# Kernel optimization log

Measured on AMD Instinct MI355X. Metric: run time of the kernel, lower is better.

Reference implementation:

```python
import jax, jax.numpy as jnp
import numpy as np

N_NODES = 50000
N_EDGES = 800000
HIDDEN = 128
EDGE_DIM = 16
N_HEADS = 8
HEAD_DIM = HIDDEN // N_HEADS
SCALE = 1.0 / np.sqrt(HEAD_DIM).astype(np.float32)
LN_EPS = 1e-5


def setup_inputs() -> dict:
    key = jax.random.key(0)
    ks = jax.random.split(key, 24)
    s = 0.02

    def w(k, shape):
        return jax.random.normal(k, shape, dtype=jnp.float32) * s

    inp = {
        "node_features": jax.random.normal(ks[0], (N_NODES, HIDDEN), dtype=jnp.float32),
        "edge_index": jax.random.randint(ks[1], (2, N_EDGES), 0, N_NODES, dtype=jnp.int32),
        "edge_features": jax.random.normal(ks[2], (N_EDGES, EDGE_DIM), dtype=jnp.float32),
        # projections stored as [in, out] (y = x @ W + b)
        "Wq": w(ks[3], (HIDDEN, HIDDEN)), "bq": jnp.zeros((HIDDEN,), jnp.float32),
        "Wk": w(ks[4], (HIDDEN, HIDDEN)), "bk": jnp.zeros((HIDDEN,), jnp.float32),
        "Wv": w(ks[5], (HIDDEN, HIDDEN)), "bv": jnp.zeros((HIDDEN,), jnp.float32),
        "Wb1": w(ks[6], (EDGE_DIM, N_HEADS)), "bb1": jnp.zeros((N_HEADS,), jnp.float32),
        "Wb2": w(ks[7], (N_HEADS, N_HEADS)), "bb2": jnp.zeros((N_HEADS,), jnp.float32),
        "Wo": w(ks[8], (HIDDEN, HIDDEN)), "bo": jnp.zeros((HIDDEN,), jnp.float32),
        "Wf1": w(ks[9], (HIDDEN, 2 * HIDDEN)), "bf1": jnp.zeros((2 * HIDDEN,), jnp.float32),
        "Wf2": w(ks[10], (2 * HIDDEN, HIDDEN)), "bf2": jnp.zeros((HIDDEN,), jnp.float32),
        "g1": jnp.ones((HIDDEN,), jnp.float32), "be1": jnp.zeros((HIDDEN,), jnp.float32),
        "g2": jnp.ones((HIDDEN,), jnp.float32), "be2": jnp.zeros((HIDDEN,), jnp.float32),
    }
    return inp


def _layer_norm(x, gamma, beta):
    mu = jnp.mean(x, axis=-1, keepdims=True)
    var = jnp.mean(jnp.square(x - mu), axis=-1, keepdims=True)
    return (x - mu) * jax.lax.rsqrt(var + LN_EPS) * gamma + beta


def reference(node_features, edge_index, edge_features,
              Wq, bq, Wk, bk, Wv, bv, Wb1, bb1, Wb2, bb2,
              Wo, bo, Wf1, bf1, Wf2, bf2, g1, be1, g2, be2):
    n_nodes = node_features.shape[0]
    src, dst = edge_index[0], edge_index[1]

    q = (node_features @ Wq + bq).reshape(n_nodes, N_HEADS, HEAD_DIM)
    k = (node_features @ Wk + bk).reshape(n_nodes, N_HEADS, HEAD_DIM)
    v = (node_features @ Wv + bv).reshape(n_nodes, N_HEADS, HEAD_DIM)

    # per-edge attention logits [E, H]
    edge_bias = jax.nn.silu(edge_features @ Wb1 + bb1) @ Wb2 + bb2
    logits = jnp.sum(q[dst] * k[src], axis=-1) * SCALE + edge_bias

    # segment softmax over edges sharing the same dst node
    max_s = jax.ops.segment_max(logits, dst, num_segments=n_nodes)
    exp_s = jnp.exp(logits - max_s[dst])
    norm = jax.ops.segment_sum(exp_s, dst, num_segments=n_nodes)
    attn = exp_s / jnp.clip(norm[dst], 1e-12)

    # weighted aggregation [N, H, D] -> [N, hidden]
    weighted = attn[:, :, None] * v[src]
    aggregated = jax.ops.segment_sum(weighted, dst, num_segments=n_nodes)
    aggregated = aggregated.reshape(n_nodes, HIDDEN)

    x = _layer_norm(node_features + (aggregated @ Wo + bo), g1, be1)
    ffn = jax.nn.silu(x @ Wf1 + bf1) @ Wf2 + bf2
    return _layer_norm(x + ffn, g2, be2)
```

## Files before the change

### kernel.cpp

```cpp
#include <hip/hip_runtime.h>
#include <hip/hip_bf16.h>
#include <math.h>

#define HIDDEN 128
#define EDGE_DIM 16
#define N_HEADS 8
#define QK_SCALE 0.25f
#define LN_EPS 1e-5f

using bf16x8 = __attribute__((ext_vector_type(8))) short;
using f32x4 = __attribute__((ext_vector_type(4))) float;
typedef __hip_bfloat16 bf16;

__device__ __forceinline__ float b2f(short u) {
  union { unsigned int i; float f; } c;
  c.i = ((unsigned int)(unsigned short)u) << 16;
  return c.f;
}
__device__ __forceinline__ short f2b(float f) {
  bf16 h = __float2bfloat16(f);
  union { bf16 b; short s; } c;
  c.b = h;
  return c.s;
}

__global__ __launch_bounds__(256) void conv_weights_kernel(
    const float* __restrict__ Wq, const float* __restrict__ Wk, const float* __restrict__ Wv,
    const float* __restrict__ bq, const float* __restrict__ bk, const float* __restrict__ bv,
    const float* __restrict__ Wo, const float* __restrict__ Wf1, const float* __restrict__ Wf2,
    bf16* __restrict__ Wqkv_t, bf16* __restrict__ Wo_t, bf16* __restrict__ Wf1_t,
    bf16* __restrict__ Wf2_t, float* __restrict__ bqkv) {
  int i = blockIdx.x * 256 + threadIdx.x;
  if (i < 49152) {
    int n = i >> 7, k = i & 127;
    const float* W = (n < 128) ? Wq : ((n < 256) ? Wk : Wv);
    int nn = n & 127;
    Wqkv_t[i] = __float2bfloat16(W[k * 128 + nn]);
  } else if (i < 65536) {
    int j = i - 49152;
    int n = j >> 7, k = j & 127;
    Wo_t[j] = __float2bfloat16(Wo[k * 128 + n]);
  } else if (i < 98304) {
    int j = i - 65536;
    int n = j >> 7, k = j & 127;
    Wf1_t[j] = __float2bfloat16(Wf1[k * 256 + n]);
  } else if (i < 131072) {
    int j = i - 98304;
    int n = j >> 8, k = j & 255;
    Wf2_t[j] = __float2bfloat16(Wf2[k * 128 + n]);
  }
  if (i < 384) bqkv[i] = (i < 128) ? bq[i] : ((i < 256) ? bk[i - 128] : bv[i - 256]);
}

template <int K, int EPI, int OUTBF, int AF32>
__global__ __launch_bounds__(256) void mfma_gemm_kernel(
    const void* __restrict__ Ap, const bf16* __restrict__ Wt,
    const float* __restrict__ bias, void* __restrict__ Cout, int M, int Nc) {
  const int tid = threadIdx.x;
  const int w = tid >> 6, l = tid & 63;
  const int wr = w >> 1, wc = w & 1;
  const int lr = l & 15, lk = l >> 4;
  const int bm = blockIdx.x * 64;
  const int bn = blockIdx.y * 128 + wc * 64;

  f32x4 acc[2][4] = {};
  const int arow0 = bm + wr * 32 + lr;

  for (int k0 = 0; k0 < K; k0 += 128) {
    bf16x8 bfr[4][4];
#pragma unroll
    for (int fn = 0; fn < 4; ++fn) {
      const bf16* wp = Wt + (size_t)(bn + fn * 16 + lr) * K + k0 + lk * 8;
#pragma unroll
      for (int ks = 0; ks < 4; ++ks) bfr[fn][ks] = *(const bf16x8*)(wp + ks * 32);
    }
    bf16x8 afr[2][4];
#pragma unroll
    for (int fr = 0; fr < 2; ++fr) {
      int row = arow0 + fr * 16;
      if (row >= M) row = M - 1;
      if (AF32) {
        const float* ap = (const float*)Ap + (size_t)row * K + k0 + lk * 8;
#pragma unroll
        for (int ks = 0; ks < 4; ++ks) {
          float4 x = *(const float4*)(ap + ks * 32);
          float4 y = *(const float4*)(ap + ks * 32 + 4);
          bf16x8 t;
          t[0] = f2b(x.x); t[1] = f2b(x.y); t[2] = f2b(x.z); t[3] = f2b(x.w);
          t[4] = f2b(y.x); t[5] = f2b(y.y); t[6] = f2b(y.z); t[7] = f2b(y.w);
          afr[fr][ks] = t;
        }
      } else {
        const bf16* ap = (const bf16*)Ap + (size_t)row * K + k0 + lk * 8;
#pragma unroll
        for (int ks = 0; ks < 4; ++ks) afr[fr][ks] = *(const bf16x8*)(ap + ks * 32);
      }
    }
#pragma unroll
    for (int ks = 0; ks < 4; ++ks)
#pragma unroll
      for (int fr = 0; fr < 2; ++fr)
#pragma unroll
        for (int fn = 0; fn < 4; ++fn)
          acc[fr][fn] = __builtin_amdgcn_mfma_f32_16x16x32_bf16(afr[fr][ks], bfr[fn][ks],
                                                                acc[fr][fn], 0, 0, 0);
  }

#pragma unroll
  for (int fn = 0; fn < 4; ++fn) {
    const int col = bn + fn * 16 + lr;
    const float bv = bias[col];
#pragma unroll
    for (int fr = 0; fr < 2; ++fr) {
      const int rbase = bm + wr * 32 + fr * 16 + lk * 4;
#pragma unroll
      for (int r = 0; r < 4; ++r) {
        int row = rbase + r;
        if (row < M) {
          float o = acc[fr][fn][r] + bv;
          if (EPI == 1) o = o / (1.f + __expf(-o));
          if (OUTBF)
            ((bf16*)Cout)[(size_t)row * Nc + col] = __float2bfloat16(o);
          else
            ((float*)Cout)[(size_t)row * Nc + col] = o;
        }
      }
    }
  }
}

template <int K>
__global__ __launch_bounds__(256) void mfma_gemm_ln_kernel(
    const bf16* __restrict__ A, const bf16* __restrict__ Wt,
    const float* __restrict__ bias, const float* __restrict__ R,
    const float* __restrict__ gam, const float* __restrict__ bet,
    float* __restrict__ y, bf16* __restrict__ yb, int M) {
  const int tid = threadIdx.x;
  const int w = tid >> 6, l = tid & 63;
  const int wr = w >> 1, wc = w & 1;
  const int lr = l & 15, lk = l >> 4;
  const int bm = blockIdx.x * 64;
  const int bn = wc * 64;

  f32x4 acc[2][4] = {};
  const int arow0 = bm + wr * 32 + lr;

  for (int k0 = 0; k0 < K; k0 += 128) {
    bf16x8 bfr[4][4];
#pragma unroll
    for (int fn = 0; fn < 4; ++fn) {
      const bf16* wp = Wt + (size_t)(bn + fn * 16 + lr) * K + k0 + lk * 8;
#pragma unroll
      for (int ks = 0; ks < 4; ++ks) bfr[fn][ks] = *(const bf16x8*)(wp + ks * 32);
    }
    bf16x8 afr[2][4];
#pragma unroll
    for (int fr = 0; fr < 2; ++fr) {
      int row = arow0 + fr * 16;
      if (row >= M) row = M - 1;
      const bf16* ap = A + (size_t)row * K + k0 + lk * 8;
#pragma unroll
      for (int ks = 0; ks < 4; ++ks) afr[fr][ks] = *(const bf16x8*)(ap + ks * 32);
    }
#pragma unroll
    for (int ks = 0; ks < 4; ++ks)
#pragma unroll
      for (int fr = 0; fr < 2; ++fr)
#pragma unroll
        for (int fn = 0; fn < 4; ++fn)
          acc[fr][fn] = __builtin_amdgcn_mfma_f32_16x16x32_bf16(afr[fr][ks], bfr[fn][ks],
                                                                acc[fr][fn], 0, 0, 0);
  }

  float bv[4], gv[4], ev[4];
#pragma unroll
  for (int fn = 0; fn < 4; ++fn) {
    int col = bn + fn * 16 + lr;
    bv[fn] = bias[col];
    gv[fn] = gam[col];
    ev[fn] = bet[col];
  }
  float ps[2][4], psq[2][4];
#pragma unroll
  for (int fr = 0; fr < 2; ++fr) {
#pragma unroll
    for (int r = 0; r < 4; ++r) {
      int row = bm + wr * 32 + fr * 16 + lk * 4 + r;
      int rrow = (row < M) ? row : (M - 1);
      float s = 0.f, sq = 0.f;
#pragma unroll
      for (int fn = 0; fn < 4; ++fn) {
        int col = bn + fn * 16 + lr;
        float o = acc[fr][fn][r] + bv[fn] + R[(size_t)rrow * HIDDEN + col];
        acc[fr][fn][r] = o;
        s += o;
        sq += o * o;
      }
      ps[fr][r] = s;
      psq[fr][r] = sq;
    }
  }
#pragma unroll
  for (int off = 1; off < 16; off <<= 1) {
#pragma unroll
    for (int fr = 0; fr < 2; ++fr)
#pragma unroll
      for (int r = 0; r < 4; ++r) {
        ps[fr][r] += __shfl_xor(ps[fr][r], off, 64);
        psq[fr][r] += __shfl_xor(psq[fr][r], off, 64);
      }
  }
  __shared__ float s_sum[2][64], s_sq[2][64];
  if (lr == 0) {
#pragma unroll
    for (int fr = 0; fr < 2; ++fr)
#pragma unroll
      for (int r = 0; r < 4; ++r) {
        int rl = wr * 32 + fr * 16 + lk * 4 + r;
        s_sum[wc][rl] = ps[fr][r];
        s_sq[wc][rl] = psq[fr][r];
      }
  }
  __syncthreads();
#pragma unroll
  for (int fr = 0; fr < 2; ++fr) {
#pragma unroll
    for (int r = 0; r < 4; ++r) {
      int rl = wr * 32 + fr * 16 + lk * 4 + r;
      int row = bm + rl;
      float tot = s_sum[0][rl] + s_sum[1][rl];
      float tsq = s_sq[0][rl] + s_sq[1][rl];
      float mean = tot * (1.f / 128.f);
      float var = tsq * (1.f / 128.f) - mean * mean;
      float rstd = rsqrtf(var + LN_EPS);
      if (row < M) {
#pragma unroll
        for (int fn = 0; fn < 4; ++fn) {
          int col = bn + fn * 16 + lr;
          float val = (acc[fr][fn][r] - mean) * rstd * gv[fn] + ev[fn];
          if (y) y[(size_t)row * HIDDEN + col] = val;
          if (yb) yb[(size_t)row * HIDDEN + col] = __float2bfloat16(val);
        }
      }
    }
  }
}

__global__ void hist_kernel(const int* __restrict__ dst, int* __restrict__ counts, int E) {
  int e = blockIdx.x * blockDim.x + threadIdx.x;
  if (e < E) atomicAdd(&counts[dst[e]], 1);
}

__device__ __forceinline__ int wave_incl_scan(int x, int lane) {
  int incl = x;
#pragma unroll
  for (int off = 1; off < 64; off <<= 1) {
    int y = __shfl_up(incl, off, 64);
    if (lane >= off) incl += y;
  }
  return incl;
}

__global__ __launch_bounds__(256) void scan_block_kernel(const int* __restrict__ counts,
                                                         int* __restrict__ offs,
                                                         int* __restrict__ btot, int N) {
  __shared__ int s4[4];
  int tid = threadIdx.x;
  int i = blockIdx.x * 256 + tid;
  int lane = tid & 63, wv = tid >> 6;
  int x = (i < N) ? counts[i] : 0;
  int incl = wave_incl_scan(x, lane);
  if (lane == 63) s4[wv] = incl;
  __syncthreads();
  if (tid == 0) {
    int s = 0;
#pragma unroll
    for (int j = 0; j < 4; ++j) { int t = s4[j]; s4[j] = s; s += t; }
    btot[blockIdx.x] = s;
  }
  __syncthreads();
  if (i < N) offs[i] = s4[wv] + incl - x;
}

__global__ __launch_bounds__(256) void scan_tot_kernel(int* __restrict__ btot, int nb) {
  __shared__ int s4[4];
  __shared__ int carry;
  int tid = threadIdx.x;
  int lane = tid & 63, wv = tid >> 6;
  if (tid == 0) carry = 0;
  __syncthreads();
  for (int c0 = 0; c0 < nb; c0 += 256) {
    int i = c0 + tid;
    int x = (i < nb) ? btot[i] : 0;
    int incl = wave_incl_scan(x, lane);
    if (lane == 63) s4[wv] = incl;
    __syncthreads();
    if (tid == 0) {
      int s = 0;
#pragma unroll
      for (int j = 0; j < 4; ++j) { int t = s4[j]; s4[j] = s; s += t; }
    }
    __syncthreads();
    int base = carry + s4[wv];
    if (i < nb) btot[i] = base + incl - x;
    __syncthreads();
    if (tid == 255) carry = base + incl;
    __syncthreads();
  }
}

__global__ __launch_bounds__(256) void scan_add_kernel(int* __restrict__ offs,
                                                       const int* __restrict__ btot,
                                                       int N, int E) {
  int i = blockIdx.x * 256 + threadIdx.x;
  if (i < N) offs[i] += btot[blockIdx.x];
  if (i == 0) offs[N] = E;
}

__global__ __launch_bounds__(256) void scatter_mlp_kernel(
    const int* __restrict__ dst, const int* __restrict__ src,
    const float* __restrict__ ef, const float* __restrict__ Wb1,
    const float* __restrict__ bb1, const float* __restrict__ Wb2,
    const float* __restrict__ bb2, const int* __restrict__ offs,
    int* __restrict__ cursor, int* __restrict__ src_csr,
    bf16* __restrict__ ebw, int E) {
  __shared__ float w1[128], w2[64], b1[8], b2[8];
  int tid = threadIdx.x;
  if (tid < 128) w1[tid] = Wb1[tid];
  else if (tid < 192) w2[tid - 128] = Wb2[tid - 128];
  else if (tid < 200) b1[tid - 192] = bb1[tid - 192];
  else if (tid < 208) b2[tid - 200] = bb2[tid - 200];
  __syncthreads();

  int e = blockIdx.x * 256 + tid;
  if (e >= E) return;

  const float4* p4 = (const float4*)(ef + (size_t)e * 16);
  float4 f0 = p4[0], f1 = p4[1], f2 = p4[2], f3 = p4[3];
  float x[16] = {f0.x, f0.y, f0.z, f0.w, f1.x, f1.y, f1.z, f1.w,
                 f2.x, f2.y, f2.z, f2.w, f3.x, f3.y, f3.z, f3.w};

  float h[8];
#pragma unroll
  for (int j = 0; j < 8; ++j) h[j] = b1[j];
#pragma unroll
  for (int i = 0; i < 16; ++i) {
    float xi = x[i];
#pragma unroll
    for (int j = 0; j < 8; ++j) h[j] = fmaf(xi, w1[i * 8 + j], h[j]);
  }
#pragma unroll
  for (int j = 0; j < 8; ++j) h[j] = h[j] / (1.f + __expf(-h[j]));

  float o[8];
#pragma unroll
  for (int j = 0; j < 8; ++j) o[j] = b2[j];
#pragma unroll
  for (int jj = 0; jj < 8; ++jj) {
    float hj = h[jj];
#pragma unroll
    for (int j = 0; j < 8; ++j) o[j] = fmaf(hj, w2[jj * 8 + j], o[j]);
  }
  bf16x8 o8;
#pragma unroll
  for (int j = 0; j < 8; ++j) o8[j] = f2b(o[j]);

  int d = dst[e];
  int p = offs[d] + atomicAdd(&cursor[d], 1);
  src_csr[p] = src[e];
  *(bf16x8*)(ebw + (size_t)p * 8) = o8;
}

__global__ __launch_bounds__(256) void node_attn_kernel(
    const bf16* __restrict__ qkv, const int* __restrict__ src_csr,
    const bf16* __restrict__ ebw, const int* __restrict__ offs,
    bf16* __restrict__ agg, int Nn) {
  int n = blockIdx.x * 4 + (threadIdx.x >> 6);
  if (n >= Nn) return;
  int l = threadIdx.x & 63;
  int g = l >> 4;
  int il = l & 15;
  int head = il >> 1;

  bf16x8 q8 = *(const bf16x8*)(qkv + (size_t)n * 384 + il * 8);
  float qf[8];
#pragma unroll
  for (int j = 0; j < 8; ++j) qf[j] = b2f(q8[j]) * QK_SCALE;

  int s0 = offs[n], s1 = offs[n + 1];
  float lsum = 0.f;
  float acc[8] = {};

  for (int p0 = s0; p0 < s1; p0 += 4) {
    int p = p0 + g;
    bool valid = p < s1;
    int pc = valid ? p : s1 - 1;
    int s = src_csr[pc];
    float ebv = b2f(ebw[(size_t)pc * 8 + head]);
    const bf16* kvrow = qkv + (size_t)s * 384 + 128;
    bf16x8 k8 = *(const bf16x8*)(kvrow + il * 8);
    bf16x8 v8 = *(const bf16x8*)(kvrow + 128 + il * 8);

    float prod = 0.f;
#pragma unroll
    for (int j = 0; j < 8; ++j) prod = fmaf(qf[j], b2f(k8[j]), prod);
    prod += __shfl_xor(prod, 1, 64);

    float pe = valid ? __expf(prod + ebv) : 0.f;
    lsum += pe;
#pragma unroll
    for (int j = 0; j < 8; ++j) acc[j] = fmaf(pe, b2f(v8[j]), acc[j]);
  }

#pragma unroll
  for (int off = 16; off < 64; off <<= 1) {
    lsum += __shfl_xor(lsum, off, 64);
#pragma unroll
    for (int j = 0; j < 8; ++j) acc[j] += __shfl_xor(acc[j], off, 64);
  }

  if (g == 0) {
    float inv = (lsum > 0.f) ? 1.f / lsum : 0.f;
    bf16x8 o8;
#pragma unroll
    for (int j = 0; j < 8; ++j) o8[j] = f2b(acc[j] * inv);
    *(bf16x8*)(agg + (size_t)n * HIDDEN + il * 8) = o8;
  }
}

extern "C" void kernel_launch(void* const* d_in, const int* in_sizes, int n_in,
                              void* d_out, int out_size, void* d_ws, size_t ws_size,
                              hipStream_t stream) {
  const float* nf = (const float*)d_in[0];
  const int* ei = (const int*)d_in[1];
  const float* ef = (const float*)d_in[2];
  const float* Wq = (const float*)d_in[3];
  const float* bq = (const float*)d_in[4];
  const float* Wk = (const float*)d_in[5];
  const float* bk_ = (const float*)d_in[6];
  const float* Wv = (const float*)d_in[7];
  const float* bv = (const float*)d_in[8];
  const float* Wb1 = (const float*)d_in[9];
  const float* bb1 = (const float*)d_in[10];
  const float* Wb2 = (const float*)d_in[11];
  const float* bb2 = (const float*)d_in[12];
  const float* Wo = (const float*)d_in[13];
  const float* bo = (const float*)d_in[14];
  const float* Wf1 = (const float*)d_in[15];
  const float* bf1 = (const float*)d_in[16];
  const float* Wf2 = (const float*)d_in[17];
  const float* bf2 = (const float*)d_in[18];
  const float* g1 = (const float*)d_in[19];
  const float* be1 = (const float*)d_in[20];
  const float* g2 = (const float*)d_in[21];
  const float* be2 = (const float*)d_in[22];

  const int N = in_sizes[0] / HIDDEN;
  const int E = in_sizes[2] / EDGE_DIM;
  const int* srcA = ei;
  const int* dstA = ei + E;

  char* base = (char*)d_ws;
  size_t off = 0;
  auto alloc = [&](size_t bytes) {
    off = (off + 255) & ~(size_t)255;
    char* p = base + off;
    off += bytes;
    return p;
  };

  bf16* qkv = (bf16*)alloc((size_t)N * 384 * 2);
  bf16* hbuf = qkv;
  bf16* agg = (bf16*)alloc((size_t)N * HIDDEN * 2);
  float* x1 = (float*)alloc((size_t)N * HIDDEN * 4);
  bf16* x1b = (bf16*)alloc((size_t)N * HIDDEN * 2);
  int* src_csr = (int*)alloc((size_t)E * 4);
  bf16* ebw = (bf16*)alloc((size_t)E * N_HEADS * 2);
  int* counts = (int*)alloc((size_t)N * 4);
  int* offs = (int*)alloc((size_t)(N + 1) * 4);
  int* cursor = (int*)alloc((size_t)N * 4);
  const int nb = (N + 255) / 256;
  int* btot = (int*)alloc((size_t)nb * 4);
  bf16* Wqkv_t = (bf16*)alloc(384 * 128 * 2);
  bf16* Wo_t = (bf16*)alloc(128 * 128 * 2);
  bf16* Wf1_t = (bf16*)alloc(256 * 128 * 2);
  bf16* Wf2_t = (bf16*)alloc(128 * 256 * 2);
  float* bqkv = (float*)alloc(384 * 4);

  float* outp = (float*)d_out;
  const int mb64 = (N + 63) / 64;
  const int eblocks = (E + 255) / 256;

  conv_weights_kernel<<<512, 256, 0, stream>>>(Wq, Wk, Wv, bq, bk_, bv, Wo, Wf1, Wf2,
                                               Wqkv_t, Wo_t, Wf1_t, Wf2_t, bqkv);

  mfma_gemm_kernel<128, 0, 1, 1><<<dim3(mb64, 3), 256, 0, stream>>>(
      nf, Wqkv_t, bqkv, qkv, N, 384);

  hipMemsetAsync(counts, 0, (size_t)N * 4, stream);
  hipMemsetAsync(cursor, 0, (size_t)N * 4, stream);
  hist_kernel<<<eblocks, 256, 0, stream>>>(dstA, counts, E);
  scan_block_kernel<<<nb, 256, 0, stream>>>(counts, offs, btot, N);
  scan_tot_kernel<<<1, 256, 0, stream>>>(btot, nb);
  scan_add_kernel<<<nb, 256, 0, stream>>>(offs, btot, N, E);
  scatter_mlp_kernel<<<eblocks, 256, 0, stream>>>(dstA, srcA, ef, Wb1, bb1, Wb2, bb2,
                                                  offs, cursor, src_csr, ebw, E);

  node_attn_kernel<<<(N + 3) / 4, 256, 0, stream>>>(qkv, src_csr, ebw, offs, agg, N);

  mfma_gemm_ln_kernel<128><<<mb64, 256, 0, stream>>>(agg, Wo_t, bo, nf, g1, be1, x1, x1b, N);

  mfma_gemm_kernel<128, 1, 1, 0><<<dim3(mb64, 2), 256, 0, stream>>>(
      x1b, Wf1_t, bf1, hbuf, N, 256);

  mfma_gemm_ln_kernel<256><<<mb64, 256, 0, stream>>>(hbuf, Wf2_t, bf2, x1, g2, be2,
                                                     outp, nullptr, N);
}
```

Baseline: 298.4 us.

## Store edge bias in edge order, widen per-lane head work, swap GEMM grid axes

The edge-bias MLP output is now written with coalesced nontemporal stores in original edge order, and the CSR stores (src, edge id) pairs so the attention kernel can gather the bias by edge id. Before, the bias was scattered to random CSR positions. The attention kernel now gives each lane a full head of 16 dims, processing 8 edges per iteration. This drops the intra-head shuffle but adds more shuffle steps for the final reduction and a random gather of the bias. GEMM grids are transposed so consecutive blocks share A rows, and the counts and cursor memsets are merged into one.

```diff
diff --git a/kernel.cpp b/kernel.cpp
--- a/kernel.cpp
+++ b/kernel.cpp
@@ -10,6 +10,7 @@
 
 using bf16x8 = __attribute__((ext_vector_type(8))) short;
 using f32x4 = __attribute__((ext_vector_type(4))) float;
+using f32x4v = __attribute__((ext_vector_type(4))) float;
 typedef __hip_bfloat16 bf16;
 
 __device__ __forceinline__ float b2f(short u) {
@@ -60,8 +61,8 @@
   const int w = tid >> 6, l = tid & 63;
   const int wr = w >> 1, wc = w & 1;
   const int lr = l & 15, lk = l >> 4;
-  const int bm = blockIdx.x * 64;
-  const int bn = blockIdx.y * 128 + wc * 64;
+  const int bm = blockIdx.y * 64;
+  const int bn = blockIdx.x * 128 + wc * 64;
 
   f32x4 acc[2][4] = {};
   const int arow0 = bm + wr * 32 + lr;
@@ -322,8 +323,8 @@
     const float* __restrict__ ef, const float* __restrict__ Wb1,
     const float* __restrict__ bb1, const float* __restrict__ Wb2,
     const float* __restrict__ bb2, const int* __restrict__ offs,
-    int* __restrict__ cursor, int* __restrict__ src_csr,
-    bf16* __restrict__ ebw, int E) {
+    int* __restrict__ cursor, int2* __restrict__ es_csr,
+    bf16* __restrict__ eb, int E) {
   __shared__ float w1[128], w2[64], b1[8], b2[8];
   int tid = threadIdx.x;
   if (tid < 128) w1[tid] = Wb1[tid];
@@ -335,10 +336,13 @@
   int e = blockIdx.x * 256 + tid;
   if (e >= E) return;
 
-  const float4* p4 = (const float4*)(ef + (size_t)e * 16);
-  float4 f0 = p4[0], f1 = p4[1], f2 = p4[2], f3 = p4[3];
-  float x[16] = {f0.x, f0.y, f0.z, f0.w, f1.x, f1.y, f1.z, f1.w,
-                 f2.x, f2.y, f2.z, f2.w, f3.x, f3.y, f3.z, f3.w};
+  const f32x4v* p4 = (const f32x4v*)(ef + (size_t)e * 16);
+  f32x4v f0 = __builtin_nontemporal_load(p4 + 0);
+  f32x4v f1 = __builtin_nontemporal_load(p4 + 1);
+  f32x4v f2 = __builtin_nontemporal_load(p4 + 2);
+  f32x4v f3 = __builtin_nontemporal_load(p4 + 3);
+  float x[16] = {f0[0], f0[1], f0[2], f0[3], f1[0], f1[1], f1[2], f1[3],
+                 f2[0], f2[1], f2[2], f2[3], f3[0], f3[1], f3[2], f3[3]};
 
   float h[8];
 #pragma unroll
@@ -364,67 +368,82 @@
   bf16x8 o8;
 #pragma unroll
   for (int j = 0; j < 8; ++j) o8[j] = f2b(o[j]);
+  __builtin_nontemporal_store(o8, (bf16x8*)(eb + (size_t)e * 8));
 
   int d = dst[e];
   int p = offs[d] + atomicAdd(&cursor[d], 1);
-  src_csr[p] = src[e];
-  *(bf16x8*)(ebw + (size_t)p * 8) = o8;
+  es_csr[p] = make_int2(src[e], e);
 }
 
 __global__ __launch_bounds__(256) void node_attn_kernel(
-    const bf16* __restrict__ qkv, const int* __restrict__ src_csr,
-    const bf16* __restrict__ ebw, const int* __restrict__ offs,
+    const bf16* __restrict__ qkv, const int2* __restrict__ es_csr,
+    const bf16* __restrict__ eb, const int* __restrict__ offs,
     bf16* __restrict__ agg, int Nn) {
   int n = blockIdx.x * 4 + (threadIdx.x >> 6);
   if (n >= Nn) return;
   int l = threadIdx.x & 63;
-  int g = l >> 4;
-  int il = l & 15;
-  int head = il >> 1;
-
-  bf16x8 q8 = *(const bf16x8*)(qkv + (size_t)n * 384 + il * 8);
-  float qf[8];
-#pragma unroll
-  for (int j = 0; j < 8; ++j) qf[j] = b2f(q8[j]) * QK_SCALE;
+  int g = l >> 3;
+  int il = l & 7;
+
+  const bf16* qrow = qkv + (size_t)n * 384 + il * 16;
+  bf16x8 qa = *(const bf16x8*)(qrow);
+  bf16x8 qb = *(const bf16x8*)(qrow + 8);
+  float qf[16];
+#pragma unroll
+  for (int j = 0; j < 8; ++j) {
+    qf[j] = b2f(qa[j]) * QK_SCALE;
+    qf[8 + j] = b2f(qb[j]) * QK_SCALE;
+  }
 
   int s0 = offs[n], s1 = offs[n + 1];
   float lsum = 0.f;
-  float acc[8] = {};
-
-  for (int p0 = s0; p0 < s1; p0 += 4) {
+  float acc[16] = {};
+
+  for (int p0 = s0; p0 < s1; p0 += 8) {
     int p = p0 + g;
     bool valid = p < s1;
     int pc = valid ? p : s1 - 1;
-    int s = src_csr[pc];
-    float ebv = b2f(ebw[(size_t)pc * 8 + head]);
-    const bf16* kvrow = qkv + (size_t)s * 384 + 128;
-    bf16x8 k8 = *(const bf16x8*)(kvrow + il * 8);
-    bf16x8 v8 = *(const bf16x8*)(kvrow + 128 + il * 8);
+    int2 es = es_csr[pc];
+    const bf16* kvrow = qkv + (size_t)es.x * 384 + 128 + il * 16;
+    bf16x8 k0 = *(const bf16x8*)(kvrow);
+    bf16x8 k1 = *(const bf16x8*)(kvrow + 8);
+    bf16x8 v0 = *(const bf16x8*)(kvrow + 128);
+    bf16x8 v1 = *(const bf16x8*)(kvrow + 136);
+    float ebv = b2f(eb[(size_t)es.y * 8 + il]);
 
     float prod = 0.f;
 #pragma unroll
-    for (int j = 0; j < 8; ++j) prod = fmaf(qf[j], b2f(k8[j]), prod);
-    prod += __shfl_xor(prod, 1, 64);
-
+    for (int j = 0; j < 8; ++j) {
+      prod = fmaf(qf[j], b2f(k0[j]), prod);
+      prod = fmaf(qf[8 + j], b2f(k1[j]), prod);
+    }
     float pe = valid ? __expf(prod + ebv) : 0.f;
     lsum += pe;
 #pragma unroll
-    for (int j = 0; j < 8; ++j) acc[j] = fmaf(pe, b2f(v8[j]), acc[j]);
-  }
-
-#pragma unroll
-  for (int off = 16; off < 64; off <<= 1) {
+    for (int j = 0; j < 8; ++j) {
+      acc[j] = fmaf(pe, b2f(v0[j]), acc[j]);
+      acc[8 + j] = fmaf(pe, b2f(v1[j]), acc[8 + j]);
+    }
+  }
+
+#pragma unroll
+  for (int off = 8; off < 64; off <<= 1) {
     lsum += __shfl_xor(lsum, off, 64);
 #pragma unroll
-    for (int j = 0; j < 8; ++j) acc[j] += __shfl_xor(acc[j], off, 64);
+    for (int j = 0; j < 16; ++j) acc[j] += __shfl_xor(acc[j], off, 64);
   }
 
   if (g == 0) {
     float inv = (lsum > 0.f) ? 1.f / lsum : 0.f;
-    bf16x8 o8;
-#pragma unroll
-    for (int j = 0; j < 8; ++j) o8[j] = f2b(acc[j] * inv);
-    *(bf16x8*)(agg + (size_t)n * HIDDEN + il * 8) = o8;
+    bf16x8 o0, o1;
+#pragma unroll
+    for (int j = 0; j < 8; ++j) {
+      o0[j] = f2b(acc[j] * inv);
+      o1[j] = f2b(acc[8 + j] * inv);
+    }
+    bf16* orow = agg + (size_t)n * HIDDEN + il * 16;
+    *(bf16x8*)(orow) = o0;
+    *(bf16x8*)(orow + 8) = o1;
   }
 }
 
@@ -474,11 +493,11 @@
   bf16* agg = (bf16*)alloc((size_t)N * HIDDEN * 2);
   float* x1 = (float*)alloc((size_t)N * HIDDEN * 4);
   bf16* x1b = (bf16*)alloc((size_t)N * HIDDEN * 2);
-  int* src_csr = (int*)alloc((size_t)E * 4);
-  bf16* ebw = (bf16*)alloc((size_t)E * N_HEADS * 2);
-  int* counts = (int*)alloc((size_t)N * 4);
+  int2* es_csr = (int2*)alloc((size_t)E * 8);
+  bf16* eb = (bf16*)alloc((size_t)E * N_HEADS * 2);
+  int* counts = (int*)alloc((size_t)N * 8);
+  int* cursor = counts + N;
   int* offs = (int*)alloc((size_t)(N + 1) * 4);
-  int* cursor = (int*)alloc((size_t)N * 4);
   const int nb = (N + 255) / 256;
   int* btot = (int*)alloc((size_t)nb * 4);
   bf16* Wqkv_t = (bf16*)alloc(384 * 128 * 2);
@@ -494,23 +513,22 @@
   conv_weights_kernel<<<512, 256, 0, stream>>>(Wq, Wk, Wv, bq, bk_, bv, Wo, Wf1, Wf2,
                                                Wqkv_t, Wo_t, Wf1_t, Wf2_t, bqkv);
 
-  mfma_gemm_kernel<128, 0, 1, 1><<<dim3(mb64, 3), 256, 0, stream>>>(
+  mfma_gemm_kernel<128, 0, 1, 1><<<dim3(3, mb64), 256, 0, stream>>>(
       nf, Wqkv_t, bqkv, qkv, N, 384);
 
-  hipMemsetAsync(counts, 0, (size_t)N * 4, stream);
-  hipMemsetAsync(cursor, 0, (size_t)N * 4, stream);
+  hipMemsetAsync(counts, 0, (size_t)N * 8, stream);
   hist_kernel<<<eblocks, 256, 0, stream>>>(dstA, counts, E);
   scan_block_kernel<<<nb, 256, 0, stream>>>(counts, offs, btot, N);
   scan_tot_kernel<<<1, 256, 0, stream>>>(btot, nb);
   scan_add_kernel<<<nb, 256, 0, stream>>>(offs, btot, N, E);
   scatter_mlp_kernel<<<eblocks, 256, 0, stream>>>(dstA, srcA, ef, Wb1, bb1, Wb2, bb2,
-                                                  offs, cursor, src_csr, ebw, E);
-
-  node_attn_kernel<<<(N + 3) / 4, 256, 0, stream>>>(qkv, src_csr, ebw, offs, agg, N);
+                                                  offs, cursor, es_csr, eb, E);
+
+  node_attn_kernel<<<(N + 3) / 4, 256, 0, stream>>>(qkv, es_csr, eb, offs, agg, N);
 
   mfma_gemm_ln_kernel<128><<<mb64, 256, 0, stream>>>(agg, Wo_t, bo, nf, g1, be1, x1, x1b, N);
 
-  mfma_gemm_kernel<128, 1, 1, 0><<<dim3(mb64, 2), 256, 0, stream>>>(
+  mfma_gemm_kernel<128, 1, 1, 0><<<dim3(2, mb64), 256, 0, stream>>>(
       x1b, Wf1_t, bf1, hbuf, N, 256);
 
   mfma_gemm_ln_kernel<256><<<mb64, 256, 0, stream>>>(hbuf, Wf2_t, bf2, x1, g2, be2,
```

Measured after the change: 308.1 us. +3.3%, slower.
